# Kernel optimization log

Measured on AMD Instinct MI355X. Metric: run time of the kernel, lower is better.

Reference implementation:

```python
import jax, jax.numpy as jnp
import numpy as np

B, N, F, C = 8, 4096, 1024, 64


def setup_inputs() -> dict:
    key = jax.random.key(0)
    k1, k2, k3 = jax.random.split(key, 3)
    x1 = jax.random.normal(k1, (B, N, F), dtype=jnp.float32)
    x2 = jax.random.normal(k2, (B, N, F), dtype=jnp.float32)
    W = jax.random.normal(k3, (C, F), dtype=jnp.float32) / np.sqrt(F)
    b = jnp.zeros((C,), dtype=jnp.float32)
    return {"x1": x1, "x2": x2, "W": W, "b": b}


def _select_max(x, W, b):
    # x: [B, N, F] -> scores [B, N, C]
    scores = jnp.einsum("bnf,cf->bnc", x, W) + b
    # per-batch, per-class index of max-scoring instance: [B, C]
    idx = jnp.argmax(scores, axis=1)
    # gather the selected instance feature vectors: [B, C, F]
    return jnp.take_along_axis(x, idx[:, :, None], axis=1)


def reference(x1, x2, W, b):
    d = _select_max(x1, W, b)
    d1 = _select_max(x2, W, b)
    return (d, d1)
```

## Files before the change

### kernel.cpp

```cpp
#include <hip/hip_runtime.h>

#define B_   8
#define N_   4096
#define F_   1024
#define C_   64
#define ROWS 64
#define KC   32
#define NT   (F_ / KC)
#define NBLK (N_ / ROWS)
#define MARGIN 0.08f

typedef __attribute__((ext_vector_type(8))) short bhalf8;
typedef __attribute__((ext_vector_type(4))) float f32x4;
typedef __attribute__((ext_vector_type(4))) unsigned short us4;

__device__ __forceinline__ unsigned short f2bf_rne(float x) {
    unsigned u = __builtin_bit_cast(unsigned, x);
    u += 0x7fffu + ((u >> 16) & 1u);
    return (unsigned short)(u >> 16);
}
__device__ __forceinline__ bhalf8 cvt8(float4 a, float4 b) {
    bhalf8 r;
    r[0] = (short)f2bf_rne(a.x); r[1] = (short)f2bf_rne(a.y);
    r[2] = (short)f2bf_rne(a.z); r[3] = (short)f2bf_rne(a.w);
    r[4] = (short)f2bf_rne(b.x); r[5] = (short)f2bf_rne(b.y);
    r[6] = (short)f2bf_rne(b.z); r[7] = (short)f2bf_rne(b.w);
    return r;
}
__device__ __forceinline__ void load_lds16(const void* g, void* l) {
    __builtin_amdgcn_global_load_lds(
        (const __attribute__((address_space(1))) unsigned int*)g,
        (__attribute__((address_space(3))) unsigned int*)l, 16, 0, 0);
}

#define LEXGT(a, ai, b, bi) ((a) > (b) || ((a) == (b) && (ai) < (bi)))
#define INSERT3(vv, nn)                                                        \
    do {                                                                       \
        float _v = (vv); int _n = (nn);                                        \
        if (LEXGT(_v, _n, v0, i0)) { v2=v1; i2=i1; v1=v0; i1=i0; v0=_v; i0=_n; } \
        else if (LEXGT(_v, _n, v1, i1)) { v2=v1; i2=i1; v1=_v; i1=_n; }        \
        else if (LEXGT(_v, _n, v2, i2)) { v2=_v; i2=_n; }                      \
    } while (0)

__global__ __launch_bounds__(256) void wconv_kernel(
    const float* __restrict__ W, unsigned short* __restrict__ Wh)
{
    int i = blockIdx.x * 256 + threadIdx.x;
    float4 v = ((const float4*)W)[i];
    us4 hh;
    hh[0] = f2bf_rne(v.x); hh[1] = f2bf_rne(v.y);
    hh[2] = f2bf_rne(v.z); hh[3] = f2bf_rne(v.w);
    ((us4*)Wh)[i] = hh;
}

__global__ __launch_bounds__(256, 4) void score_top_kernel(
    const float* __restrict__ x1, const float* __restrict__ x2,
    const unsigned short* __restrict__ Wh,
    float* __restrict__ pv, int* __restrict__ pi)
{
    __shared__ __align__(16) char lds[24576];

    const int tid  = threadIdx.x;
    const int nb   = blockIdx.x;
    const int b    = blockIdx.y;
    const int inp  = blockIdx.z;
    const float* __restrict__ x = inp ? x2 : x1;
    const float* __restrict__ xbase = x + ((size_t)b * N_ + (size_t)nb * ROWS) * F_;

    const int lane = tid & 63;
    const int w    = tid >> 6;
    const int rsel = lane & 15;
    const int g    = lane >> 4;

#define XOFF(buf) ((buf) * 8192)
#define WOFF(buf) (16384 + (buf) * 4096)

#define STAGE(t, buf)                                                          \
    do {                                                                       \
        const int f0_ = (t) * KC;                                              \
        _Pragma("unroll")                                                      \
        for (int j = 0; j < 2; ++j) {                                          \
            int ii = w * 2 + j;                                                \
            int r  = ii * 8 + (lane >> 3);                                     \
            int cg = (lane & 7) ^ (r & 7);                                     \
            load_lds16(xbase + (size_t)r * F_ + f0_ + cg * 4,                  \
                       lds + XOFF(buf) + ii * 1024);                           \
        }                                                                      \
        {                                                                      \
            int cls = w * 16 + (lane >> 2);                                    \
            int cg  = (lane & 3) ^ ((cls >> 1) & 3);                           \
            load_lds16(Wh + (size_t)cls * F_ + f0_ + cg * 8,                   \
                       lds + WOFF(buf) + w * 1024);                            \
        }                                                                      \
    } while (0)

    f32x4 acc[4];
    #pragma unroll
    for (int nt = 0; nt < 4; ++nt) acc[nt] = (f32x4){0.f, 0.f, 0.f, 0.f};

    const int r_    = w * 16 + rsel;
    const int aswz0 = ((2 * g)     ^ (r_ & 7)) * 16;
    const int aswz1 = ((2 * g + 1) ^ (r_ & 7)) * 16;

    STAGE(0, 0);
    __syncthreads();

    for (int t = 0; t < NT; ++t) {
        const int cur = t & 1;
        if (t + 1 < NT) STAGE(t + 1, cur ^ 1);

        const char* xb = lds + XOFF(cur);
        const char* wb = lds + WOFF(cur);
        float4 xlo = *(const float4*)(xb + r_ * 128 + aswz0);
        float4 xhi = *(const float4*)(xb + r_ * 128 + aswz1);
        bhalf8 ah = cvt8(xlo, xhi);
        #pragma unroll
        for (int nt = 0; nt < 4; ++nt) {
            int cls = nt * 16 + rsel;
            bhalf8 bf = *(const bhalf8*)(wb + cls * 64 + ((g ^ ((cls >> 1) & 3)) * 16));
            acc[nt] = __builtin_amdgcn_mfma_f32_16x16x32_bf16(ah, bf, acc[nt], 0, 0, 0);
        }
        __syncthreads();
    }

    float wv0[4], wv1[4], wv2[4]; int wi0[4], wi1[4], wi2[4];
    #pragma unroll
    for (int nt = 0; nt < 4; ++nt) {
        float v0 = -3.4e38f, v1 = -3.4e38f, v2 = -3.4e38f;
        int   i0 = 0x7fffffff, i1 = 0x7fffffff, i2 = 0x7fffffff;
        #pragma unroll
        for (int r = 0; r < 4; ++r) {
            int n = nb * ROWS + w * 16 + 4 * g + r;
            INSERT3(acc[nt][r], n);
        }
        #pragma unroll
        for (int d = 16; d <= 32; d <<= 1) {
            float u0 = __shfl_xor(v0, d), u1 = __shfl_xor(v1, d), u2 = __shfl_xor(v2, d);
            int   j0 = __shfl_xor(i0, d), j1 = __shfl_xor(i1, d), j2 = __shfl_xor(i2, d);
            INSERT3(u0, j0); INSERT3(u1, j1); INSERT3(u2, j2);
        }
        wv0[nt] = v0; wv1[nt] = v1; wv2[nt] = v2;
        wi0[nt] = i0; wi1[nt] = i1; wi2[nt] = i2;
    }

    __syncthreads();
    float* tv = (float*)lds;
    int*   ti = (int*)(lds + 8192);
    if (lane < 16) {
        #pragma unroll
        for (int nt = 0; nt < 4; ++nt) {
            int c = nt * 16 + lane;
            tv[(w * C_ + c) * 3 + 0] = wv0[nt]; ti[(w * C_ + c) * 3 + 0] = wi0[nt];
            tv[(w * C_ + c) * 3 + 1] = wv1[nt]; ti[(w * C_ + c) * 3 + 1] = wi1[nt];
            tv[(w * C_ + c) * 3 + 2] = wv2[nt]; ti[(w * C_ + c) * 3 + 2] = wi2[nt];
        }
    }
    __syncthreads();

    if (tid < C_) {
        int c = tid;
        float v0 = -3.4e38f, v1 = -3.4e38f, v2 = -3.4e38f;
        int   i0 = 0x7fffffff, i1 = 0x7fffffff, i2 = 0x7fffffff;
        #pragma unroll
        for (int ww = 0; ww < 4; ++ww)
            #pragma unroll
            for (int k = 0; k < 3; ++k)
                INSERT3(tv[(ww * C_ + c) * 3 + k], ti[(ww * C_ + c) * 3 + k]);
        int blk = ((inp * B_ + b) * NBLK + nb);
        pv[(blk * C_ + c) * 3 + 0] = v0; pi[(blk * C_ + c) * 3 + 0] = i0;
        pv[(blk * C_ + c) * 3 + 1] = v1; pi[(blk * C_ + c) * 3 + 1] = i1;
        pv[(blk * C_ + c) * 3 + 2] = v2; pi[(blk * C_ + c) * 3 + 2] = i2;
    }
}

__global__ __launch_bounds__(256) void select_gather_kernel(
    const float* __restrict__ x1, const float* __restrict__ x2,
    const float* __restrict__ W,
    const float* __restrict__ pv, const int* __restrict__ pi,
    float* __restrict__ out)
{
    const int c   = blockIdx.x;
    const int b   = blockIdx.y;
    const int inp = blockIdx.z;
    const int tid = threadIdx.x;

    __shared__ int   s_cnt;
    __shared__ float s_m[4];
    __shared__ int   s_cand[16];
    __shared__ float s_val[16];
    __shared__ float s_wsum[4];
    __shared__ int   s_win;

    if (tid == 0) s_cnt = 0;
    __syncthreads();

    float v = -3.4e38f; int id = 0;
    if (tid < NBLK * 3) {
        int nbk = tid / 3, k = tid - nbk * 3;
        int blk = ((inp * B_ + b) * NBLK + nbk);
        int off = (blk * C_ + c) * 3 + k;
        v = pv[off]; id = pi[off];
    }
    {
        float m = v;
        #pragma unroll
        for (int d = 32; d; d >>= 1) m = fmaxf(m, __shfl_xor(m, d));
        if ((tid & 63) == 0) s_m[tid >> 6] = m;
    }
    __syncthreads();
    const float m = fmaxf(fmaxf(s_m[0], s_m[1]), fmaxf(s_m[2], s_m[3]));
    if (v >= m - MARGIN) {
        int p = atomicAdd(&s_cnt, 1);
        if (p < 16) s_cand[p] = id;
    }
    __syncthreads();

    const float* __restrict__ x = inp ? x2 : x1;
    const int ncand = min(s_cnt, 16);
    int winner;
    if (ncand == 1) {
        winner = s_cand[0];
    } else {
        for (int k = 0; k < ncand; ++k) {
            int n = s_cand[k];
            float4 xv = *(const float4*)(x + ((size_t)b * N_ + n) * F_ + tid * 4);
            float4 wq = *(const float4*)(W + (size_t)c * F_ + tid * 4);
            float p = xv.x * wq.x + xv.y * wq.y + xv.z * wq.z + xv.w * wq.w;
            #pragma unroll
            for (int d = 32; d; d >>= 1) p += __shfl_down(p, d);
            if ((tid & 63) == 0) s_wsum[tid >> 6] = p;
            __syncthreads();
            if (tid == 0) s_val[k] = s_wsum[0] + s_wsum[1] + s_wsum[2] + s_wsum[3];
            __syncthreads();
        }
        if (tid == 0) {
            float bv = s_val[0]; int bn = s_cand[0];
            for (int k = 1; k < ncand; ++k)
                if (s_val[k] > bv || (s_val[k] == bv && s_cand[k] < bn)) { bv = s_val[k]; bn = s_cand[k]; }
            s_win = bn;
        }
        __syncthreads();
        winner = s_win;
    }

    float4 vv = *(const float4*)(x + ((size_t)b * N_ + winner) * F_ + tid * 4);
    *(float4*)(out + (((size_t)inp * B_ + b) * C_ + c) * F_ + tid * 4) = vv;
}

extern "C" void kernel_launch(void* const* d_in, const int* in_sizes, int n_in,
                              void* d_out, int out_size, void* d_ws, size_t ws_size,
                              hipStream_t stream) {
    const float* x1 = (const float*)d_in[0];
    const float* x2 = (const float*)d_in[1];
    const float* W  = (const float*)d_in[2];

    unsigned short* Wh = (unsigned short*)d_ws;
    float* pv = (float*)((char*)d_ws + (size_t)C_ * F_ * sizeof(unsigned short));
    int*   pi = (int*)((char*)pv + (size_t)2 * B_ * NBLK * C_ * 3 * sizeof(float));

    wconv_kernel<<<C_ * F_ / 1024, 256, 0, stream>>>(W, Wh);
    dim3 g1(NBLK, B_, 2);
    score_top_kernel<<<g1, 256, 0, stream>>>(x1, x2, Wh, pv, pi);
    dim3 g2(C_, B_, 2);
    select_gather_kernel<<<g2, 256, 0, stream>>>(x1, x2, W, pv, pi, (float*)d_out);
}
```

Measured before the change: 65.98 us.

## Triple-buffer LDS staging with explicit vmcnt waits instead of double buffering

```diff
diff --git a/kernel.cpp b/kernel.cpp
--- a/kernel.cpp
+++ b/kernel.cpp
@@ -58,7 +58,7 @@
     const unsigned short* __restrict__ Wh,
     float* __restrict__ pv, int* __restrict__ pi)
 {
-    __shared__ __align__(16) char lds[24576];
+    __shared__ __align__(16) char lds[36864];
 
     const int tid  = threadIdx.x;
     const int nb   = blockIdx.x;
@@ -73,7 +73,7 @@
     const int g    = lane >> 4;
 
 #define XOFF(buf) ((buf) * 8192)
-#define WOFF(buf) (16384 + (buf) * 4096)
+#define WOFF(buf) (24576 + (buf) * 4096)
 
 #define STAGE(t, buf)                                                          \
     do {                                                                       \
@@ -92,6 +92,22 @@
             load_lds16(Wh + (size_t)cls * F_ + f0_ + cg * 8,                   \
                        lds + WOFF(buf) + w * 1024);                            \
         }                                                                      \
+        __builtin_amdgcn_sched_barrier(0);                                     \
+    } while (0)
+
+#define COMPUTE(buf)                                                           \
+    do {                                                                       \
+        const char* xb = lds + XOFF(buf);                                      \
+        const char* wb = lds + WOFF(buf);                                      \
+        float4 xlo = *(const float4*)(xb + r_ * 128 + aswz0);                  \
+        float4 xhi = *(const float4*)(xb + r_ * 128 + aswz1);                  \
+        bhalf8 ah = cvt8(xlo, xhi);                                            \
+        _Pragma("unroll")                                                      \
+        for (int nt = 0; nt < 4; ++nt) {                                       \
+            int cls = nt * 16 + rsel;                                          \
+            bhalf8 bf = *(const bhalf8*)(wb + cls * 64 + ((g ^ ((cls >> 1) & 3)) * 16)); \
+            acc[nt] = __builtin_amdgcn_mfma_f32_16x16x32_bf16(ah, bf, acc[nt], 0, 0, 0); \
+        }                                                                      \
     } while (0)
 
     f32x4 acc[4];
@@ -103,25 +119,25 @@
     const int aswz1 = ((2 * g + 1) ^ (r_ & 7)) * 16;
 
     STAGE(0, 0);
-    __syncthreads();
-
-    for (int t = 0; t < NT; ++t) {
-        const int cur = t & 1;
-        if (t + 1 < NT) STAGE(t + 1, cur ^ 1);
-
-        const char* xb = lds + XOFF(cur);
-        const char* wb = lds + WOFF(cur);
-        float4 xlo = *(const float4*)(xb + r_ * 128 + aswz0);
-        float4 xhi = *(const float4*)(xb + r_ * 128 + aswz1);
-        bhalf8 ah = cvt8(xlo, xhi);
-        #pragma unroll
-        for (int nt = 0; nt < 4; ++nt) {
-            int cls = nt * 16 + rsel;
-            bhalf8 bf = *(const bhalf8*)(wb + cls * 64 + ((g ^ ((cls >> 1) & 3)) * 16));
-            acc[nt] = __builtin_amdgcn_mfma_f32_16x16x32_bf16(ah, bf, acc[nt], 0, 0, 0);
-        }
-        __syncthreads();
-    }
+    STAGE(1, 1);
+
+    for (int t = 0; t < NT - 2; ++t) {
+        STAGE(t + 2, (t + 2) % 3);
+        asm volatile("s_waitcnt vmcnt(6)" ::: "memory");
+        __builtin_amdgcn_s_barrier();
+        __builtin_amdgcn_sched_barrier(0);
+        COMPUTE(t % 3);
+        __builtin_amdgcn_sched_barrier(0);
+        __builtin_amdgcn_s_barrier();
+    }
+    asm volatile("s_waitcnt vmcnt(3)" ::: "memory");
+    __builtin_amdgcn_s_barrier();
+    __builtin_amdgcn_sched_barrier(0);
+    COMPUTE((NT - 2) % 3);
+    asm volatile("s_waitcnt vmcnt(0)" ::: "memory");
+    __builtin_amdgcn_s_barrier();
+    __builtin_amdgcn_sched_barrier(0);
+    COMPUTE((NT - 1) % 3);
 
     float wv0[4], wv1[4], wv2[4]; int wi0[4], wi1[4], wi2[4];
     #pragma unroll
```

Result: no change. 66.11 us (+0.2%).
